# Optimization experiments

Hardware: AMD Instinct MI355X
Metric: run time of the kernel (lower is better)

Reference implementation:

```python
import jax, jax.numpy as jnp
import numpy as np

BATCH, C_IN, C_OUT, N_GRID, N_MODES = 64, 64, 64, 8192, 64
SCALE = 1.0 / (C_IN * C_OUT)


def setup_inputs() -> dict:
    key = jax.random.key(0)
    k1, k2, k3 = jax.random.split(key, 3)
    lhss = jax.random.normal(k1, (BATCH, C_IN, N_GRID), dtype=jnp.float32)
    # torch.rand on cfloat draws real and imag uniformly in [0,1), then scaled
    w_real = SCALE * jax.random.uniform(k2, (C_IN, C_OUT, N_MODES), dtype=jnp.float32)
    w_imag = SCALE * jax.random.uniform(k3, (C_IN, C_OUT, N_MODES), dtype=jnp.float32)
    return {"lhss": lhss, "w_real": w_real, "w_imag": w_imag}


def reference(lhss, w_real, w_imag):
    n = lhss.shape[-1]
    n_freq = n // 2 + 1  # rfft output length
    weights = w_real + 1j * w_imag  # (c_in, c_out, modes), complex64
    xf = jnp.fft.rfft(lhss)  # (b, c_in, n_freq) complex
    # complex channel-mixing on the first N_MODES frequency bins only
    mixed = jnp.einsum("bix,iox->box", xf[:, :, :N_MODES], weights)
    # zero-pad remaining high-frequency bins, then inverse rfft
    res = jnp.zeros((lhss.shape[0], weights.shape[1], n_freq), dtype=mixed.dtype)
    res = res.at[:, :, :N_MODES].set(mixed)
    return jnp.fft.irfft(res, n=n)
```

## Files before the change

kernel.cpp:

```cpp
#include <hip/hip_runtime.h>
#include <hip/hip_bf16.h>

#define NG 8192
#define NB 64
#define CI 64
#define CO 64
#define NM 64
#define NFJ 128
#define NROWS 4096

typedef __bf16 bf16x8 __attribute__((ext_vector_type(8)));
typedef float f32x4 __attribute__((ext_vector_type(4)));

#define GLOAD_LDS16(gsrc, ldst)                                                   \
    __builtin_amdgcn_global_load_lds(                                             \
        (const __attribute__((address_space(1))) void*)(gsrc),                    \
        (__attribute__((address_space(3))) void*)(ldst), 16, 0, 0)


__global__ __launch_bounds__(256) void sc_prep(const float* __restrict__ wr,
                                               const float* __restrict__ wi,
                                               __bf16* __restrict__ Ft,
                                               __bf16* __restrict__ Ginv,
                                               __bf16* __restrict__ Wtf) {
    const float W0 = 6.2831853071795864769f / (float)NG;
    if (blockIdx.x < 8192) {
        int idx = blockIdx.x * 256 + threadIdx.x;
        if (idx < 128 * NG) {
            int j = idx >> 13, pos = idx & (NG - 1);
            int blk = pos >> 6, g = (pos >> 3) & 7, e = pos & 7;
            int ksrc = (blk << 6) + (((g ^ (j & 7)) << 3) | e);
            int m = j >> 1;
            int t = (m * ksrc) & (NG - 1);
            float s, c;
            __sincosf((float)t * W0, &s, &c);
            Ft[idx] = (__bf16)((j & 1) ? -s : c);
        } else {
            int i2 = idx - 128 * NG;
            int n = i2 >> 7, pos = i2 & 127;
            int g = pos >> 3, e = pos & 7;
            int psrc = ((g ^ (n & 15)) << 3) | e;
            int m = psrc >> 1, im = psrc & 1;
            int t = (m * n) & (NG - 1);
            float s, c;
            __sincosf((float)t * W0, &s, &c);
            float v;
            if (im) v = (m == 0) ? 0.0f : (-2.0f / NG) * s;
            else    v = ((m == 0) ? 1.0f : 2.0f) / NG * c;
            Ginv[i2] = (__bf16)v;
        }
    } else {
        const int i = blockIdx.x - 8192, t = threadIdx.x;
        const int o = t & 63, kq = t >> 6;
        float wrk[16], wik[16];
        const float* pr = wr + ((size_t)i * 64 + o) * 64 + kq * 16;
        const float* pq = wi + ((size_t)i * 64 + o) * 64 + kq * 16;
        #pragma unroll
        for (int m = 0; m < 4; ++m) {
            float4 a = *(const float4*)(pr + m * 4);
            float4 b = *(const float4*)(pq + m * 4);
            wrk[m*4+0]=a.x; wrk[m*4+1]=a.y; wrk[m*4+2]=a.z; wrk[m*4+3]=a.w;
            wik[m*4+0]=b.x; wik[m*4+1]=b.y; wik[m*4+2]=b.z; wik[m*4+3]=b.w;
        }
        const int ks_a = i >> 5, ks_b = 2 + (i >> 5);
        const int kg = (i >> 3) & 3, e = i & 7, ot = o >> 4, l = o & 15;
        const int pos = (kg * 16 + l) * 8 + e;
        #pragma unroll
        for (int kk = 0; kk < 16; ++kk) {
            int k = kq * 16 + kk;
            Wtf[(size_t)(((k*2+0)*4+ks_a)*4+ot)*512 + pos] = (__bf16)wrk[kk];
            Wtf[(size_t)(((k*2+0)*4+ks_b)*4+ot)*512 + pos] = (__bf16)(-wik[kk]);
            Wtf[(size_t)(((k*2+1)*4+ks_a)*4+ot)*512 + pos] = (__bf16)wik[kk];
            Wtf[(size_t)(((k*2+1)*4+ks_b)*4+ot)*512 + pos] = (__bf16)wrk[kk];
        }
    }
}

__global__ __launch_bounds__(256) void sc_dft(const float* __restrict__ A,
                                              const __bf16* __restrict__ Ft,
                                              float* __restrict__ XFp,
                                              int nsteps) {
    __shared__ __align__(16) char smem[49152];
    char* A0 = smem;
    char* A1 = smem + 8192;
    char* F0 = smem + 16384;
    char* F1 = smem + 32768;

    const int tid = threadIdx.x;
    const int w = tid >> 6, lane = tid & 63;
    const int l15 = lane & 15, kg = lane >> 4;
    const int wm = w >> 1, wn = w & 1;
    const int rt = blockIdx.x & 63, sp = blockIdx.x >> 6;
    const int r0 = rt * 64;
    const size_t kb0 = (size_t)sp * nsteps * 64;
    const int swz = l15 & 7;

    float4 av[4];
    f32x4 acc[2][4] = {};

    auto issueA = [&](int step) {
        size_t kb = kb0 + (size_t)step * 64;
        #pragma unroll
        for (int s = 0; s < 4; ++s) {
            int c = s * 256 + tid;
            av[s] = *(const float4*)(A + (size_t)(r0 + (c >> 4)) * NG + kb + (c & 15) * 4);
        }
    };
    auto writeA = [&](char* Ab) {
        #pragma unroll
        for (int s = 0; s < 4; ++s) {
            int c = s * 256 + tid, row = c >> 4, cq = c & 15;
            union { __bf16 h[4]; uint2 u; } cv;
            cv.h[0] = (__bf16)av[s].x; cv.h[1] = (__bf16)av[s].y;
            cv.h[2] = (__bf16)av[s].z; cv.h[3] = (__bf16)av[s].w;
            *(uint2*)(Ab + row * 128 + (((cq >> 1) ^ (row & 7)) << 4) + ((cq & 1) << 3)) = cv.u;
        }
    };
    auto stageF = [&](int step, char* Fb) {
        size_t kb = kb0 + (size_t)step * 64;
        #pragma unroll
        for (int s = 0; s < 4; ++s) {
            int cc = s * 256 + tid;
            GLOAD_LDS16(Ft + (size_t)(cc >> 3) * NG + kb + (cc & 7) * 8, Fb + cc * 16);
        }
    };
    auto compute = [&](const char* Ab, const char* Fb) {
        #pragma unroll
        for (int ks2 = 0; ks2 < 2; ++ks2) {
            bf16x8 a[2], b[4];
            #pragma unroll
            for (int mt = 0; mt < 2; ++mt)
                a[mt] = *(const bf16x8*)(Ab + (wm*32 + mt*16 + l15) * 128 +
                                         (((ks2*4 + kg) ^ swz) << 4));
            #pragma unroll
            for (int jt = 0; jt < 4; ++jt)
                b[jt] = *(const bf16x8*)(Fb + (wn*64 + jt*16 + l15) * 128 +
                                         (((ks2*4 + kg) ^ swz) << 4));
            #pragma unroll
            for (int mt = 0; mt < 2; ++mt)
                #pragma unroll
                for (int jt = 0; jt < 4; ++jt)
                    acc[mt][jt] = __builtin_amdgcn_mfma_f32_16x16x32_bf16(
                        a[mt], b[jt], acc[mt][jt], 0, 0, 0);
        }
    };

    issueA(0); stageF(0, F0); writeA(A0);
    __syncthreads();
    for (int t = 0; t < nsteps; ++t) {
        char* Ac = (t & 1) ? A1 : A0;
        char* Fc = (t & 1) ? F1 : F0;
        char* An = (t & 1) ? A0 : A1;
        char* Fn = (t & 1) ? F0 : F1;
        if (t + 1 < nsteps) { issueA(t + 1); stageF(t + 1, Fn); }
        compute(Ac, Fc);
        if (t + 1 < nsteps) writeA(An);
        __syncthreads();
    }
    #pragma unroll
    for (int mt = 0; mt < 2; ++mt)
        #pragma unroll
        for (int jt = 0; jt < 4; ++jt)
            *(f32x4*)(XFp + ((size_t)sp * NFJ + wn*64 + jt*16 + l15) * NROWS +
                      (r0 + wm*32 + mt*16 + kg*4)) = acc[mt][jt];
}

__global__ __launch_bounds__(256) void sc_mix(const float* __restrict__ XFp,
                                              const __bf16* __restrict__ Wtf,
                                              __bf16* __restrict__ M2, int nsplit) {
    __shared__ __align__(16) char at[4096];
    const int t = threadIdx.x;
    const int k = blockIdx.x >> 2, bq = blockIdx.x & 3;
    const int lane = t & 63, ot = t >> 6;
    const int l15 = lane & 15, kg = lane >> 4;

    const int c = t >> 7, t127 = t & 127;
    f32x4 s0 = {}, s1 = {};
    {
        const float* src = XFp + (size_t)(2*k + c) * NROWS + bq*1024 + t127*8;
        const size_t pstride = (size_t)NFJ * NROWS;
        if (nsplit == 8) {
            #pragma unroll
            for (int p = 0; p < 8; ++p) {
                s0 += *(const f32x4*)(src + p*pstride);
                s1 += *(const f32x4*)(src + p*pstride + 4);
            }
        } else {
            for (int p = 0; p < nsplit; ++p) {
                s0 += *(const f32x4*)(src + p*pstride);
                s1 += *(const f32x4*)(src + p*pstride + 4);
            }
        }
    }
    {
        const int bl = t127 >> 3;
        const int i0 = (t127 & 7) * 8;
        union { __bf16 h[8]; uint4 u; } cv;
        cv.h[0]=(__bf16)s0[0]; cv.h[1]=(__bf16)s0[1];
        cv.h[2]=(__bf16)s0[2]; cv.h[3]=(__bf16)s0[3];
        cv.h[4]=(__bf16)s1[0]; cv.h[5]=(__bf16)s1[1];
        cv.h[6]=(__bf16)s1[2]; cv.h[7]=(__bf16)s1[3];
        *(uint4*)(at + bl*256 + ((((c*64 + i0) >> 3) ^ bl) << 4)) = cv.u;
    }
    __syncthreads();

    bf16x8 a[4];
    #pragma unroll
    for (int ks = 0; ks < 4; ++ks)
        a[ks] = *(const bf16x8*)(at + l15*256 + (((ks*4 + kg) ^ l15) << 4));

    f32x4 accR = {}, accI = {};
    #pragma unroll
    for (int ks = 0; ks < 4; ++ks) {
        bf16x8 b0 = *(const bf16x8*)(Wtf + (size_t)(((k*2+0)*4+ks)*4+ot)*512 + lane*8);
        accR = __builtin_amdgcn_mfma_f32_16x16x32_bf16(a[ks], b0, accR, 0, 0, 0);
    }
    #pragma unroll
    for (int ks = 0; ks < 4; ++ks) {
        bf16x8 b1 = *(const bf16x8*)(Wtf + (size_t)(((k*2+1)*4+ks)*4+ot)*512 + lane*8);
        accI = __builtin_amdgcn_mfma_f32_16x16x32_bf16(a[ks], b1, accI, 0, 0, 0);
    }
    #pragma unroll
    for (int rr = 0; rr < 4; ++rr) {
        int bg = bq*16 + kg*4 + rr;
        size_t r = (size_t)bg * CO + ot*16 + l15;
        ushort2 pk;
        pk.x = __builtin_bit_cast(unsigned short, (__bf16)accR[rr]);
        pk.y = __builtin_bit_cast(unsigned short, (__bf16)accI[rr]);
        *(ushort2*)(M2 + r * NFJ + 2 * k) = pk;
    }
}

__global__ __launch_bounds__(512) void sc_idft(const __bf16* __restrict__ M2,
                                               const __bf16* __restrict__ Ginv,
                                               float* __restrict__ out) {
    __shared__ __align__(16) char gls[32768];
    const int tid = threadIdx.x;
    const int w = tid >> 6, lane = tid & 63;
    const int l15 = lane & 15, kg = lane >> 4;
    const int wm = w >> 1;
    const int wn = w & 1;
    const int r0 = (blockIdx.x >> 6) * 128;
    const int n0 = (blockIdx.x & 63) * 128;

    #pragma unroll
    for (int s = 0; s < 4; ++s) {
        int cc = s * 512 + tid;
        GLOAD_LDS16(Ginv + (size_t)n0 * NFJ + cc * 8, gls + cc * 16);
    }

    bf16x8 af[2][4];
    #pragma unroll
    for (int mt = 0; mt < 2; ++mt)
        #pragma unroll
        for (int ks = 0; ks < 4; ++ks)
            af[mt][ks] = *(const bf16x8*)(M2 + (size_t)(r0 + wm*32 + mt*16 + l15) * NFJ +
                                          ks*32 + kg*8);
    __syncthreads();

    f32x4 acc[2][4] = {};
    #pragma unroll
    for (int nt = 0; nt < 4; ++nt) {
        int row = wn*64 + nt*16 + l15;
        bf16x8 bfr[4];
        #pragma unroll
        for (int ks = 0; ks < 4; ++ks)
            bfr[ks] = *(const bf16x8*)(gls + row * 256 + (((ks*4 + kg) ^ (row & 15)) << 4));
        #pragma unroll
        for (int mt = 0; mt < 2; ++mt)
            #pragma unroll
            for (int ks = 0; ks < 4; ++ks)
                acc[mt][nt] = __builtin_amdgcn_mfma_f32_16x16x32_bf16(
                    af[mt][ks], bfr[ks], acc[mt][nt], 0, 0, 0);
    }
    #pragma unroll
    for (int mt = 0; mt < 2; ++mt)
        #pragma unroll
        for (int nt = 0; nt < 4; ++nt)
            #pragma unroll
            for (int rr = 0; rr < 4; ++rr)
                out[(size_t)(r0 + wm*32 + mt*16 + kg*4 + rr) * NG +
                    n0 + wn*64 + nt*16 + l15] = acc[mt][nt][rr];
}

extern "C" void kernel_launch(void* const* d_in, const int* in_sizes, int n_in,
                              void* d_out, int out_size, void* d_ws, size_t ws_size,
                              hipStream_t stream) {
    const float* lhss = (const float*)d_in[0];
    const float* w_real = (const float*)d_in[1];
    const float* w_imag = (const float*)d_in[2];
    float* out = (float*)d_out;

    char* ws = (char*)d_ws;
    __bf16* Ft_sw   = (__bf16*)ws;
    __bf16* Ginv_sw = (__bf16*)(ws + (2u << 20));
    __bf16* M2      = (__bf16*)(ws + (6u << 20));
    __bf16* Wtf     = (__bf16*)(ws + (7u << 20));
    float*  XFp     = (float*) (ws + (9u << 20));

    int split;
    if      (ws_size >= (25u << 20)) split = 8;
    else if (ws_size >= (17u << 20)) split = 4;
    else if (ws_size >= (13u << 20)) split = 2;
    else                             split = 1;
    int nsteps = 128 / split;

    sc_prep<<<8256, 256, 0, stream>>>(w_real, w_imag, Ft_sw, Ginv_sw, Wtf);
    sc_dft<<<64 * split, 256, 0, stream>>>(lhss, Ft_sw, XFp, nsteps);
    sc_mix<<<256, 256, 0, stream>>>(XFp, Wtf, M2, split);
    sc_idft<<<2048, 512, 0, stream>>>(M2, Ginv_sw, out);
}
```

Measured before the change: 88.42 us.

## Halve DFT row tile, stage weight transpose via LDS, vectorize IDFT output stores

The forward DFT kernel drops from 64-row to 32-row tiles and launches twice as many blocks, so more CUs are busy for the split-K GEMM, at the cost of reloading the twiddle matrix more often. The weight-prep path now has one block per mode, builds that mode's transposed complex weight tile in LDS and writes it out with coalesced 16-byte stores instead of scattered 2-byte global stores. The inverse DFT swaps MFMA operand order so each lane holds four contiguous output columns, which allows float4 stores in place of strided scalar stores.

```diff
diff --git a/kernel.cpp b/kernel.cpp
--- a/kernel.cpp
+++ b/kernel.cpp
@@ -23,9 +23,10 @@
                                                __bf16* __restrict__ Ft,
                                                __bf16* __restrict__ Ginv,
                                                __bf16* __restrict__ Wtf) {
+    __shared__ __align__(16) __bf16 wlds[16384];
     const float W0 = 6.2831853071795864769f / (float)NG;
-    if (blockIdx.x < 8192) {
-        int idx = blockIdx.x * 256 + threadIdx.x;
+    if (blockIdx.x >= 64) {
+        int idx = (blockIdx.x - 64) * 256 + threadIdx.x;
         if (idx < 128 * NG) {
             int j = idx >> 13, pos = idx & (NG - 1);
             int blk = pos >> 6, g = (pos >> 3) & 7, e = pos & 7;
@@ -50,29 +51,34 @@
             Ginv[i2] = (__bf16)v;
         }
     } else {
-        const int i = blockIdx.x - 8192, t = threadIdx.x;
-        const int o = t & 63, kq = t >> 6;
-        float wrk[16], wik[16];
-        const float* pr = wr + ((size_t)i * 64 + o) * 64 + kq * 16;
-        const float* pq = wi + ((size_t)i * 64 + o) * 64 + kq * 16;
-        #pragma unroll
-        for (int m = 0; m < 4; ++m) {
-            float4 a = *(const float4*)(pr + m * 4);
-            float4 b = *(const float4*)(pq + m * 4);
-            wrk[m*4+0]=a.x; wrk[m*4+1]=a.y; wrk[m*4+2]=a.z; wrk[m*4+3]=a.w;
-            wik[m*4+0]=b.x; wik[m*4+1]=b.y; wik[m*4+2]=b.z; wik[m*4+3]=b.w;
-        }
-        const int ks_a = i >> 5, ks_b = 2 + (i >> 5);
-        const int kg = (i >> 3) & 3, e = i & 7, ot = o >> 4, l = o & 15;
-        const int pos = (kg * 16 + l) * 8 + e;
-        #pragma unroll
-        for (int kk = 0; kk < 16; ++kk) {
-            int k = kq * 16 + kk;
-            Wtf[(size_t)(((k*2+0)*4+ks_a)*4+ot)*512 + pos] = (__bf16)wrk[kk];
-            Wtf[(size_t)(((k*2+0)*4+ks_b)*4+ot)*512 + pos] = (__bf16)(-wik[kk]);
-            Wtf[(size_t)(((k*2+1)*4+ks_a)*4+ot)*512 + pos] = (__bf16)wik[kk];
-            Wtf[(size_t)(((k*2+1)*4+ks_b)*4+ot)*512 + pos] = (__bf16)wrk[kk];
-        }
+        const int m = blockIdx.x;
+        const int t = threadIdx.x;
+        const int o = t & 63, q = t >> 6;
+        const int ot = o >> 4, l = o & 15;
+        float wrv[16], wiv[16];
+        #pragma unroll
+        for (int cc = 0; cc < 16; ++cc) {
+            int ci = q * 16 + cc;
+            wrv[cc] = wr[((size_t)ci * 64 + o) * 64 + m];
+            wiv[cc] = wi[((size_t)ci * 64 + o) * 64 + m];
+        }
+        #pragma unroll
+        for (int cc = 0; cc < 16; ++cc) {
+            int ci = q * 16 + cc;
+            int ksa = ci >> 5, ksb = 2 + ksa;
+            int kg = (ci >> 3) & 3, e = ci & 7;
+            int pos = (kg * 16 + l) * 8 + e;
+            wlds[(0*16 + ksa*4 + ot)*512 + pos] = (__bf16)wrv[cc];
+            wlds[(0*16 + ksb*4 + ot)*512 + pos] = (__bf16)(-wiv[cc]);
+            wlds[(1*16 + ksa*4 + ot)*512 + pos] = (__bf16)wiv[cc];
+            wlds[(1*16 + ksb*4 + ot)*512 + pos] = (__bf16)wrv[cc];
+        }
+        __syncthreads();
+        const uint4* src = (const uint4*)wlds;
+        uint4* dst = (uint4*)(Wtf + (size_t)m * 16384);
+        #pragma unroll
+        for (int s = 0; s < 8; ++s)
+            dst[s * 256 + t] = src[s * 256 + t];
     }
 }
 
@@ -80,35 +86,35 @@
                                               const __bf16* __restrict__ Ft,
                                               float* __restrict__ XFp,
                                               int nsteps) {
-    __shared__ __align__(16) char smem[49152];
+    __shared__ __align__(16) char smem[40960];
     char* A0 = smem;
-    char* A1 = smem + 8192;
-    char* F0 = smem + 16384;
-    char* F1 = smem + 32768;
+    char* A1 = smem + 4096;
+    char* F0 = smem + 8192;
+    char* F1 = smem + 24576;
 
     const int tid = threadIdx.x;
     const int w = tid >> 6, lane = tid & 63;
     const int l15 = lane & 15, kg = lane >> 4;
     const int wm = w >> 1, wn = w & 1;
-    const int rt = blockIdx.x & 63, sp = blockIdx.x >> 6;
-    const int r0 = rt * 64;
+    const int rt = blockIdx.x & 127, sp = blockIdx.x >> 7;
+    const int r0 = rt * 32;
     const size_t kb0 = (size_t)sp * nsteps * 64;
     const int swz = l15 & 7;
 
-    float4 av[4];
-    f32x4 acc[2][4] = {};
+    float4 av[2];
+    f32x4 acc[4] = {};
 
     auto issueA = [&](int step) {
         size_t kb = kb0 + (size_t)step * 64;
         #pragma unroll
-        for (int s = 0; s < 4; ++s) {
+        for (int s = 0; s < 2; ++s) {
             int c = s * 256 + tid;
             av[s] = *(const float4*)(A + (size_t)(r0 + (c >> 4)) * NG + kb + (c & 15) * 4);
         }
     };
     auto writeA = [&](char* Ab) {
         #pragma unroll
-        for (int s = 0; s < 4; ++s) {
+        for (int s = 0; s < 2; ++s) {
             int c = s * 256 + tid, row = c >> 4, cq = c & 15;
             union { __bf16 h[4]; uint2 u; } cv;
             cv.h[0] = (__bf16)av[s].x; cv.h[1] = (__bf16)av[s].y;
@@ -127,21 +133,17 @@
     auto compute = [&](const char* Ab, const char* Fb) {
         #pragma unroll
         for (int ks2 = 0; ks2 < 2; ++ks2) {
-            bf16x8 a[2], b[4];
-            #pragma unroll
-            for (int mt = 0; mt < 2; ++mt)
-                a[mt] = *(const bf16x8*)(Ab + (wm*32 + mt*16 + l15) * 128 +
-                                         (((ks2*4 + kg) ^ swz) << 4));
+            bf16x8 a, b[4];
+            a = *(const bf16x8*)(Ab + (wm*16 + l15) * 128 +
+                                 (((ks2*4 + kg) ^ swz) << 4));
             #pragma unroll
             for (int jt = 0; jt < 4; ++jt)
                 b[jt] = *(const bf16x8*)(Fb + (wn*64 + jt*16 + l15) * 128 +
                                          (((ks2*4 + kg) ^ swz) << 4));
             #pragma unroll
-            for (int mt = 0; mt < 2; ++mt)
-                #pragma unroll
-                for (int jt = 0; jt < 4; ++jt)
-                    acc[mt][jt] = __builtin_amdgcn_mfma_f32_16x16x32_bf16(
-                        a[mt], b[jt], acc[mt][jt], 0, 0, 0);
+            for (int jt = 0; jt < 4; ++jt)
+                acc[jt] = __builtin_amdgcn_mfma_f32_16x16x32_bf16(
+                    a, b[jt], acc[jt], 0, 0, 0);
         }
     };
 
@@ -158,11 +160,9 @@
         __syncthreads();
     }
     #pragma unroll
-    for (int mt = 0; mt < 2; ++mt)
-        #pragma unroll
-        for (int jt = 0; jt < 4; ++jt)
-            *(f32x4*)(XFp + ((size_t)sp * NFJ + wn*64 + jt*16 + l15) * NROWS +
-                      (r0 + wm*32 + mt*16 + kg*4)) = acc[mt][jt];
+    for (int jt = 0; jt < 4; ++jt)
+        *(f32x4*)(XFp + ((size_t)sp * NFJ + wn*64 + jt*16 + l15) * NROWS +
+                  (r0 + wm*16 + kg*4)) = acc[jt];
 }
 
 __global__ __launch_bounds__(256) void sc_mix(const float* __restrict__ XFp,
@@ -271,16 +271,14 @@
             #pragma unroll
             for (int ks = 0; ks < 4; ++ks)
                 acc[mt][nt] = __builtin_amdgcn_mfma_f32_16x16x32_bf16(
-                    af[mt][ks], bfr[ks], acc[mt][nt], 0, 0, 0);
+                    bfr[ks], af[mt][ks], acc[mt][nt], 0, 0, 0);
     }
     #pragma unroll
     for (int mt = 0; mt < 2; ++mt)
         #pragma unroll
         for (int nt = 0; nt < 4; ++nt)
-            #pragma unroll
-            for (int rr = 0; rr < 4; ++rr)
-                out[(size_t)(r0 + wm*32 + mt*16 + kg*4 + rr) * NG +
-                    n0 + wn*64 + nt*16 + l15] = acc[mt][nt][rr];
+            *(f32x4*)(out + (size_t)(r0 + wm*32 + mt*16 + l15) * NG +
+                      n0 + wn*64 + nt*16 + kg*4) = acc[mt][nt];
 }
 
 extern "C" void kernel_launch(void* const* d_in, const int* in_sizes, int n_in,
@@ -306,7 +304,7 @@
     int nsteps = 128 / split;
 
     sc_prep<<<8256, 256, 0, stream>>>(w_real, w_imag, Ft_sw, Ginv_sw, Wtf);
-    sc_dft<<<64 * split, 256, 0, stream>>>(lhss, Ft_sw, XFp, nsteps);
+    sc_dft<<<128 * split, 256, 0, stream>>>(lhss, Ft_sw, XFp, nsteps);
     sc_mix<<<256, 256, 0, stream>>>(XFp, Wtf, M2, split);
     sc_idft<<<2048, 512, 0, stream>>>(M2, Ginv_sw, out);
 }
```

Measured after the change: 105.8 us. +19.6%, slower.
